# Optimization experiments

Hardware: AMD Instinct MI355X
Metric: run time of the kernel (lower is better)

Reference implementation:

```python
import jax, jax.numpy as jnp
import numpy as np


def setup_inputs() -> dict:
    key = jax.random.key(0)
    k1, k2 = jax.random.split(key)
    B, Cin, H, W = 32, 32, 128, 128
    Cout, K = 64, 3
    inp = jax.random.normal(k1, (B, Cin, H, W), dtype=jnp.float32)
    # Original stores out_c*in_c*k*k scalar params; equivalent dense weight [Cout, Cin, K, K]
    kernel = jax.random.normal(k2, (Cout, Cin, K, K), dtype=jnp.float32)
    return {"input": inp, "kernel": kernel}


def reference(input, kernel):
    # Stride-1 cross-correlation with 'same' zero padding of (K-1)//2, identical
    # to the nested-loop slice/multiply/sum in the torch module.
    K = kernel.shape[-1]
    pad = (K - 1) // 2
    out = jax.lax.conv_general_dilated(
        input, kernel,
        window_strides=(1, 1),
        padding=[(pad, pad), (pad, pad)],
        dimension_numbers=("NCHW", "OIHW", "NCHW"),
    )
    return out  # [B, Cout, H, W]
```

## Files before the change

kernel.cpp:

```cpp
#include <hip/hip_runtime.h>
#include <hip/hip_bf16.h>
#include <stdint.h>

typedef short bf16x8 __attribute__((ext_vector_type(8)));
typedef float f32x4  __attribute__((ext_vector_type(4)));

#define B_   32
#define CIN  32
#define COUT 64
#define H_   128
#define W_   128
#define HW   (H_ * W_)
#define T_   2
#define RROWS 4
#define PXW  130

static __device__ __forceinline__ ushort f2bf(float v) {
    union { float f; uint32_t u; } cv; cv.f = v;
    uint32_t u = cv.u;
    uint32_t r = (u + 0x7FFFu + ((u >> 16) & 1u)) >> 16;
    return (ushort)r;
}

__global__ void prep_w_kernel(const float* __restrict__ wt, ushort* __restrict__ Wp) {
    int p = blockIdx.x * blockDim.x + threadIdx.x;
    if (p >= COUT * CIN * 9) return;
    int j    = p & 7;
    int lane = (p >> 3) & 63;
    int g    = (p >> 9) & 3;
    int tap  = p >> 11;
    int oc   = g * 16 + (lane & 15);
    int cin  = (lane >> 4) * 8 + j;
    int ky   = tap / 3;
    int kx   = tap % 3;
    Wp[p] = f2bf(wt[(((size_t)oc * CIN + cin) * 3 + ky) * 3 + kx]);
}

__global__ __launch_bounds__(256, 4) void conv_fused_kernel(
    const float* __restrict__ in, const ushort* __restrict__ Wp,
    float* __restrict__ out) {
    __shared__ ushort lds[RROWS * PXW * 32];

    int hw_blk  = blockIdx.x;
    int logical = (hw_blk & 7) * 256 + (hw_blk >> 3);
    int b   = logical >> 6;
    int h0  = (logical & 63) * T_;
    int tid = threadIdx.x;

    for (int i = tid; i < RROWS * PXW; i += 256) {
        int r  = i / PXW;
        int px = i - r * PXW;
        int gy = h0 + r - 1;
        bf16x8 v[4];
        if (gy >= 0 && gy < H_ && px >= 1 && px <= W_) {
            const float* src = in + ((size_t)b * CIN * H_ + gy) * W_ + (px - 1);
#pragma unroll
            for (int q = 0; q < 4; ++q)
#pragma unroll
                for (int j = 0; j < 8; ++j)
                    v[q][j] = (short)f2bf(src[(size_t)(q * 8 + j) * HW]);
        } else {
#pragma unroll
            for (int q = 0; q < 4; ++q)
#pragma unroll
                for (int j = 0; j < 8; ++j)
                    v[q][j] = 0;
        }
        uint32_t base_byte = (uint32_t)i * 64;
        uint32_t sw = ((uint32_t)(px >> 1) & 3u) << 4;
#pragma unroll
        for (int q = 0; q < 4; ++q)
            *(bf16x8*)((char*)lds + base_byte + (((uint32_t)q << 4) ^ sw)) = v[q];
    }
    __syncthreads();

    int wid  = tid >> 6;
    int lane = tid & 63;
    int llo  = lane & 15;
    int lhi  = lane >> 4;
    int row  = wid >> 1;
    int px0  = (wid & 1) * 64;
    int h    = h0 + row;

    f32x4 acc[4][4];
#pragma unroll
    for (int g = 0; g < 4; ++g)
#pragma unroll
        for (int nf = 0; nf < 4; ++nf) {
            acc[g][nf][0] = 0.f; acc[g][nf][1] = 0.f;
            acc[g][nf][2] = 0.f; acc[g][nf][3] = 0.f;
        }

#pragma unroll
    for (int tap = 0; tap < 9; ++tap) {
        int dy = tap / 3;
        int dx = tap % 3;
        int rbase = (row + dy) * PXW;
#pragma unroll
        for (int nf = 0; nf < 4; ++nf) {
            int px = px0 + nf * 16 + llo + dx;
            uint32_t byte = (uint32_t)(rbase + px) * 64u +
                            (((uint32_t)lhi << 4) ^ ((((uint32_t)px >> 1) & 3u) << 4));
            bf16x8 Bf = *(const bf16x8*)((const char*)lds + byte);
#pragma unroll
            for (int g = 0; g < 4; ++g) {
                bf16x8 Af = *(const bf16x8*)(Wp + ((size_t)(tap * 4 + g) * 64 + lane) * 8);
                acc[g][nf] = __builtin_amdgcn_mfma_f32_16x16x32_bf16(Af, Bf, acc[g][nf], 0, 0, 0);
            }
        }
    }

    float* obase = out + (size_t)b * COUT * HW + (size_t)h * W_;
#pragma unroll
    for (int g = 0; g < 4; ++g)
#pragma unroll
        for (int nf = 0; nf < 4; ++nf) {
            int x = px0 + nf * 16 + llo;
#pragma unroll
            for (int r = 0; r < 4; ++r) {
                int oc = g * 16 + lhi * 4 + r;
                obase[(size_t)oc * HW + x] = acc[g][nf][r];
            }
        }
}

__global__ void conv_naive_kernel(const float* __restrict__ in,
                                  const float* __restrict__ wt,
                                  float* __restrict__ out) {
    int idx = blockIdx.x * blockDim.x + threadIdx.x;
    if (idx >= B_ * COUT * HW) return;
    int w  = idx & 127;
    int h  = (idx >> 7) & 127;
    int oc = (idx >> 14) & 63;
    int b  = idx >> 20;
    float s = 0.f;
    for (int c = 0; c < CIN; ++c)
        for (int ky = 0; ky < 3; ++ky) {
            int y = h + ky - 1;
            if ((unsigned)y >= (unsigned)H_) continue;
            for (int kx = 0; kx < 3; ++kx) {
                int x = w + kx - 1;
                if ((unsigned)x >= (unsigned)W_) continue;
                s += in[((size_t)(b * CIN + c) * H_ + y) * W_ + x] *
                     wt[(((size_t)oc * CIN + c) * 3 + ky) * 3 + kx];
            }
        }
    out[idx] = s;
}

extern "C" void kernel_launch(void* const* d_in, const int* in_sizes, int n_in,
                              void* d_out, int out_size, void* d_ws, size_t ws_size,
                              hipStream_t stream) {
    const float* in = (const float*)d_in[0];
    const float* wt = (const float*)d_in[1];
    float* out = (float*)d_out;

    size_t Wp_bytes = (size_t)COUT * CIN * 9 * 2;

    if (ws_size >= Wp_bytes) {
        ushort* Wp = (ushort*)d_ws;
        prep_w_kernel<<<(COUT * CIN * 9 + 255) / 256, 256, 0, stream>>>(wt, Wp);
        conv_fused_kernel<<<B_ * (H_ / T_), 256, 0, stream>>>(in, Wp, out);
    } else {
        int total = B_ * COUT * HW;
        conv_naive_kernel<<<(total + 255) / 256, 256, 0, stream>>>(in, wt, out);
    }
}
```

Baseline: 52.70 us.

## Split conv accumulation into two pixel halves with nontemporal output stores

Result: slower. 59.47 us (+12.8%).

```diff
diff --git a/kernel.cpp b/kernel.cpp
--- a/kernel.cpp
+++ b/kernel.cpp
@@ -16,10 +16,8 @@
 #define PXW  130
 
 static __device__ __forceinline__ ushort f2bf(float v) {
-    union { float f; uint32_t u; } cv; cv.f = v;
-    uint32_t u = cv.u;
-    uint32_t r = (u + 0x7FFFu + ((u >> 16) & 1u)) >> 16;
-    return (ushort)r;
+    __hip_bfloat16 h = __float2bfloat16(v);
+    return __builtin_bit_cast(ushort, h);
 }
 
 __global__ void prep_w_kernel(const float* __restrict__ wt, ushort* __restrict__ Wp) {
@@ -81,47 +79,52 @@
     int row  = wid >> 1;
     int px0  = (wid & 1) * 64;
     int h    = h0 + row;
+    float* obase = out + (size_t)b * COUT * HW + (size_t)h * W_;
 
-    f32x4 acc[4][4];
 #pragma unroll
-    for (int g = 0; g < 4; ++g)
+    for (int half = 0; half < 2; ++half) {
+        f32x4 acc[4][2];
 #pragma unroll
-        for (int nf = 0; nf < 4; ++nf) {
-            acc[g][nf][0] = 0.f; acc[g][nf][1] = 0.f;
-            acc[g][nf][2] = 0.f; acc[g][nf][3] = 0.f;
+        for (int g = 0; g < 4; ++g)
+#pragma unroll
+            for (int q = 0; q < 2; ++q) {
+                acc[g][q][0] = 0.f; acc[g][q][1] = 0.f;
+                acc[g][q][2] = 0.f; acc[g][q][3] = 0.f;
+            }
+
+#pragma unroll
+        for (int tap = 0; tap < 9; ++tap) {
+            int dy = tap / 3;
+            int dx = tap % 3;
+            int rbase = (row + dy) * PXW;
+            bf16x8 Af[4];
+#pragma unroll
+            for (int g = 0; g < 4; ++g)
+                Af[g] = *(const bf16x8*)(Wp + ((size_t)(tap * 4 + g) * 64 + lane) * 8);
+#pragma unroll
+            for (int q = 0; q < 2; ++q) {
+                int px = px0 + (half * 2 + q) * 16 + llo + dx;
+                uint32_t byte = (uint32_t)(rbase + px) * 64u +
+                                (((uint32_t)lhi << 4) ^ ((((uint32_t)px >> 1) & 3u) << 4));
+                bf16x8 Bf = *(const bf16x8*)((const char*)lds + byte);
+#pragma unroll
+                for (int g = 0; g < 4; ++g)
+                    acc[g][q] = __builtin_amdgcn_mfma_f32_16x16x32_bf16(Af[g], Bf, acc[g][q], 0, 0, 0);
+            }
         }
 
 #pragma unroll
-    for (int tap = 0; tap < 9; ++tap) {
-        int dy = tap / 3;
-        int dx = tap % 3;
-        int rbase = (row + dy) * PXW;
+        for (int g = 0; g < 4; ++g)
 #pragma unroll
-        for (int nf = 0; nf < 4; ++nf) {
-            int px = px0 + nf * 16 + llo + dx;
-            uint32_t byte = (uint32_t)(rbase + px) * 64u +
-                            (((uint32_t)lhi << 4) ^ ((((uint32_t)px >> 1) & 3u) << 4));
-            bf16x8 Bf = *(const bf16x8*)((const char*)lds + byte);
+            for (int q = 0; q < 2; ++q) {
+                int x = px0 + (half * 2 + q) * 16 + llo;
 #pragma unroll
-            for (int g = 0; g < 4; ++g) {
-                bf16x8 Af = *(const bf16x8*)(Wp + ((size_t)(tap * 4 + g) * 64 + lane) * 8);
-                acc[g][nf] = __builtin_amdgcn_mfma_f32_16x16x32_bf16(Af, Bf, acc[g][nf], 0, 0, 0);
+                for (int r = 0; r < 4; ++r) {
+                    int oc = g * 16 + lhi * 4 + r;
+                    __builtin_nontemporal_store(acc[g][q][r], &obase[(size_t)oc * HW + x]);
+                }
             }
-        }
     }
-
-    float* obase = out + (size_t)b * COUT * HW + (size_t)h * W_;
-#pragma unroll
-    for (int g = 0; g < 4; ++g)
-#pragma unroll
-        for (int nf = 0; nf < 4; ++nf) {
-            int x = px0 + nf * 16 + llo;
-#pragma unroll
-            for (int r = 0; r < 4; ++r) {
-                int oc = g * 16 + lhi * 4 + r;
-                obase[(size_t)oc * HW + x] = acc[g][nf][r];
-            }
-        }
 }
 
 __global__ void conv_naive_kernel(const float* __restrict__ in,
```

## Pipeline conv over 8-row bands with rolling LDS ring and prefetch

Applied to the files above, without the earlier changes.

Measured after the change: 142.1 us. 2.7x slower.

```diff
diff --git a/kernel.cpp b/kernel.cpp
--- a/kernel.cpp
+++ b/kernel.cpp
@@ -5,21 +5,21 @@
 typedef short bf16x8 __attribute__((ext_vector_type(8)));
 typedef float f32x4  __attribute__((ext_vector_type(4)));
 
-#define B_   32
-#define CIN  32
-#define COUT 64
-#define H_   128
-#define W_   128
-#define HW   (H_ * W_)
-#define T_   2
-#define RROWS 4
-#define PXW  130
+#define B_    32
+#define CIN   32
+#define COUT  64
+#define H_    128
+#define W_    128
+#define HW    (H_ * W_)
+#define PXW   130
+#define SLOTS 6
+#define ROWS_PER_BLK 8
+#define TILES 4
+#define NBLK  512
 
 static __device__ __forceinline__ ushort f2bf(float v) {
-    union { float f; uint32_t u; } cv; cv.f = v;
-    uint32_t u = cv.u;
-    uint32_t r = (u + 0x7FFFu + ((u >> 16) & 1u)) >> 16;
-    return (ushort)r;
+    __hip_bfloat16 h = __float2bfloat16(v);
+    return __builtin_bit_cast(ushort, h);
 }
 
 __global__ void prep_w_kernel(const float* __restrict__ wt, ushort* __restrict__ Wp) {
@@ -36,41 +36,54 @@
     Wp[p] = f2bf(wt[(((size_t)oc * CIN + cin) * 3 + ky) * 3 + kx]);
 }
 
-__global__ __launch_bounds__(256, 4) void conv_fused_kernel(
+__global__ __launch_bounds__(256, 2) void conv_pipe_kernel(
     const float* __restrict__ in, const ushort* __restrict__ Wp,
     float* __restrict__ out) {
-    __shared__ ushort lds[RROWS * PXW * 32];
+    __shared__ ushort lds[SLOTS * PXW * 32];
 
     int hw_blk  = blockIdx.x;
-    int logical = (hw_blk & 7) * 256 + (hw_blk >> 3);
-    int b   = logical >> 6;
-    int h0  = (logical & 63) * T_;
+    int logical = (hw_blk & 7) * (NBLK / 8) + (hw_blk >> 3);
+    int b   = logical >> 4;
+    int bh0 = (logical & 15) * ROWS_PER_BLK;
     int tid = threadIdx.x;
 
-    for (int i = tid; i < RROWS * PXW; i += 256) {
-        int r  = i / PXW;
-        int px = i - r * PXW;
-        int gy = h0 + r - 1;
-        bf16x8 v[4];
-        if (gy >= 0 && gy < H_ && px >= 1 && px <= W_) {
-            const float* src = in + ((size_t)b * CIN * H_ + gy) * W_ + (px - 1);
-#pragma unroll
-            for (int q = 0; q < 4; ++q)
-#pragma unroll
-                for (int j = 0; j < 8; ++j)
-                    v[q][j] = (short)f2bf(src[(size_t)(q * 8 + j) * HW]);
+    const float* ib = in + (size_t)b * CIN * HW;
+
+    if (tid < 2 * SLOTS) {
+        int s  = tid >> 1;
+        int px = (tid & 1) ? (PXW - 1) : 0;
+        char* base = (char*)lds + (uint32_t)(s * PXW + px) * 64u;
+        bf16x8 z = (bf16x8)0;
+#pragma unroll
+        for (int q = 0; q < 4; ++q) *(bf16x8*)(base + q * 16) = z;
+    }
+
+#pragma unroll
+    for (int c0 = 0; c0 < 2; ++c0) {
+        int c  = c0 * 256 + tid;
+        int rr = c >> 7;
+        int px = 1 + (c & 127);
+        int p  = bh0 + rr;
+        int gy = p - 1;
+        float v[32];
+        if (gy >= 0 && gy < H_) {
+            const float* src = ib + (size_t)gy * W_ + (px - 1);
+#pragma unroll
+            for (int ch = 0; ch < 32; ++ch) v[ch] = src[(size_t)ch * HW];
         } else {
 #pragma unroll
-            for (int q = 0; q < 4; ++q)
-#pragma unroll
-                for (int j = 0; j < 8; ++j)
-                    v[q][j] = 0;
-        }
-        uint32_t base_byte = (uint32_t)i * 64;
-        uint32_t sw = ((uint32_t)(px >> 1) & 3u) << 4;
-#pragma unroll
-        for (int q = 0; q < 4; ++q)
-            *(bf16x8*)((char*)lds + base_byte + (((uint32_t)q << 4) ^ sw)) = v[q];
+            for (int ch = 0; ch < 32; ++ch) v[ch] = 0.f;
+        }
+        int slot = p % SLOTS;
+        uint32_t base = (uint32_t)(slot * PXW + px) * 64u;
+        uint32_t sw = (((uint32_t)px >> 1) & 3u) << 4;
+#pragma unroll
+        for (int q = 0; q < 4; ++q) {
+            bf16x8 w;
+#pragma unroll
+            for (int j = 0; j < 8; ++j) w[j] = (short)f2bf(v[q * 8 + j]);
+            *(bf16x8*)((char*)lds + base + (((uint32_t)q << 4) ^ sw)) = w;
+        }
     }
     __syncthreads();
 
@@ -80,48 +93,83 @@
     int lhi  = lane >> 4;
     int row  = wid >> 1;
     int px0  = (wid & 1) * 64;
-    int h    = h0 + row;
-
-    f32x4 acc[4][4];
-#pragma unroll
-    for (int g = 0; g < 4; ++g)
-#pragma unroll
-        for (int nf = 0; nf < 4; ++nf) {
-            acc[g][nf][0] = 0.f; acc[g][nf][1] = 0.f;
-            acc[g][nf][2] = 0.f; acc[g][nf][3] = 0.f;
-        }
-
-#pragma unroll
-    for (int tap = 0; tap < 9; ++tap) {
-        int dy = tap / 3;
-        int dx = tap % 3;
-        int rbase = (row + dy) * PXW;
-#pragma unroll
-        for (int nf = 0; nf < 4; ++nf) {
-            int px = px0 + nf * 16 + llo + dx;
-            uint32_t byte = (uint32_t)(rbase + px) * 64u +
-                            (((uint32_t)lhi << 4) ^ ((((uint32_t)px >> 1) & 3u) << 4));
-            bf16x8 Bf = *(const bf16x8*)((const char*)lds + byte);
-#pragma unroll
-            for (int g = 0; g < 4; ++g) {
-                bf16x8 Af = *(const bf16x8*)(Wp + ((size_t)(tap * 4 + g) * 64 + lane) * 8);
-                acc[g][nf] = __builtin_amdgcn_mfma_f32_16x16x32_bf16(Af, Bf, acc[g][nf], 0, 0, 0);
-            }
-        }
-    }
-
-    float* obase = out + (size_t)b * COUT * HW + (size_t)h * W_;
-#pragma unroll
-    for (int g = 0; g < 4; ++g)
-#pragma unroll
-        for (int nf = 0; nf < 4; ++nf) {
-            int x = px0 + nf * 16 + llo;
-#pragma unroll
-            for (int r = 0; r < 4; ++r) {
-                int oc = g * 16 + lhi * 4 + r;
-                obase[(size_t)oc * HW + x] = acc[g][nf][r];
-            }
-        }
+
+    int st_rr = tid >> 7;
+    int st_px = 1 + (tid & 127);
+
+    for (int t = 0; t < TILES; ++t) {
+        int h0t = bh0 + 2 * t;
+
+        int  sp   = h0t + 4 + st_rr;
+        int  sgy  = sp - 1;
+        bool zero = (sgy >= H_);
+        int  gy_e = zero ? 0 : sgy;
+        const float* src = ib + (size_t)gy_e * W_ + (st_px - 1);
+        float stv[32];
+#pragma unroll
+        for (int ch = 0; ch < 32; ++ch) stv[ch] = src[(size_t)ch * HW];
+
+        f32x4 acc[4][4];
+#pragma unroll
+        for (int g = 0; g < 4; ++g)
+#pragma unroll
+            for (int nf = 0; nf < 4; ++nf) {
+                acc[g][nf][0] = 0.f; acc[g][nf][1] = 0.f;
+                acc[g][nf][2] = 0.f; acc[g][nf][3] = 0.f;
+            }
+
+#pragma unroll
+        for (int tap = 0; tap < 9; ++tap) {
+            int dy = tap / 3;
+            int dx = tap % 3;
+            int p  = h0t + row + dy;
+            int rbase = (p % SLOTS) * PXW;
+            bf16x8 Af[4];
+#pragma unroll
+            for (int g = 0; g < 4; ++g)
+                Af[g] = *(const bf16x8*)(Wp + ((size_t)(tap * 4 + g) * 64 + lane) * 8);
+#pragma unroll
+            for (int nf = 0; nf < 4; ++nf) {
+                int px = px0 + nf * 16 + llo + dx;
+                uint32_t byte = (uint32_t)(rbase + px) * 64u +
+                                (((uint32_t)lhi << 4) ^ ((((uint32_t)px >> 1) & 3u) << 4));
+                bf16x8 Bf = *(const bf16x8*)((const char*)lds + byte);
+#pragma unroll
+                for (int g = 0; g < 4; ++g)
+                    acc[g][nf] = __builtin_amdgcn_mfma_f32_16x16x32_bf16(Af[g], Bf, acc[g][nf], 0, 0, 0);
+            }
+        }
+
+        if (t < TILES - 1) {
+            int slot = sp % SLOTS;
+            uint32_t base = (uint32_t)(slot * PXW + st_px) * 64u;
+            uint32_t sw = (((uint32_t)st_px >> 1) & 3u) << 4;
+#pragma unroll
+            for (int q = 0; q < 4; ++q) {
+                bf16x8 w;
+#pragma unroll
+                for (int j = 0; j < 8; ++j)
+                    w[j] = zero ? (short)0 : (short)f2bf(stv[q * 8 + j]);
+                *(bf16x8*)((char*)lds + base + (((uint32_t)q << 4) ^ sw)) = w;
+            }
+        }
+
+        int h = h0t + row;
+        float* obase = out + (size_t)b * COUT * HW + (size_t)h * W_;
+#pragma unroll
+        for (int g = 0; g < 4; ++g)
+#pragma unroll
+            for (int nf = 0; nf < 4; ++nf) {
+                int x = px0 + nf * 16 + llo;
+#pragma unroll
+                for (int r = 0; r < 4; ++r) {
+                    int oc = g * 16 + lhi * 4 + r;
+                    obase[(size_t)oc * HW + x] = acc[g][nf][r];
+                }
+            }
+
+        __syncthreads();
+    }
 }
 
 __global__ void conv_naive_kernel(const float* __restrict__ in,
@@ -160,7 +208,7 @@
     if (ws_size >= Wp_bytes) {
         ushort* Wp = (ushort*)d_ws;
         prep_w_kernel<<<(COUT * CIN * 9 + 255) / 256, 256, 0, stream>>>(wt, Wp);
-        conv_fused_kernel<<<B_ * (H_ / T_), 256, 0, stream>>>(in, Wp, out);
+        conv_pipe_kernel<<<NBLK, 256, 0, stream>>>(in, Wp, out);
     } else {
         int total = B_ * COUT * HW;
         conv_naive_kernel<<<(total + 255) / 256, 256, 0, stream>>>(in, wt, out);
```
